# Kernel tuning notes

Hardware: AMD Instinct MI355X
Metric: run time of the kernel (lower is better)

## Reference

```python
import jax, jax.numpy as jnp
import numpy as np

N_NODES = 100000
N_EDGES = 1600000
NODE_DIM = 64
EDGE_DIM = 16
HIDDEN_DIM = 64


def setup_inputs() -> dict:
    key = jax.random.key(0)
    ks = jax.random.split(key, 9)
    x = jax.random.normal(ks[0], (N_NODES, NODE_DIM), dtype=jnp.float32)
    edge_index = jax.random.randint(ks[1], (2, N_EDGES), 0, N_NODES, dtype=jnp.int32)
    edge_attr = jax.random.normal(ks[2], (N_EDGES, EDGE_DIM), dtype=jnp.float32)
    msg_in = 2 * NODE_DIM + EDGE_DIM
    s1 = 1.0 / np.sqrt(msg_in)
    s2 = 1.0 / np.sqrt(HIDDEN_DIM)
    su = 1.0 / np.sqrt(NODE_DIM + HIDDEN_DIM)
    W1 = jax.random.uniform(ks[3], (msg_in, HIDDEN_DIM), jnp.float32, -s1, s1)
    b1 = jax.random.uniform(ks[4], (HIDDEN_DIM,), jnp.float32, -s1, s1)
    W2 = jax.random.uniform(ks[5], (HIDDEN_DIM, HIDDEN_DIM), jnp.float32, -s2, s2)
    b2 = jax.random.uniform(ks[6], (HIDDEN_DIM,), jnp.float32, -s2, s2)
    Wu = jax.random.uniform(ks[7], (NODE_DIM + HIDDEN_DIM, NODE_DIM), jnp.float32, -su, su)
    bu = jax.random.uniform(ks[8], (NODE_DIM,), jnp.float32, -su, su)
    return {"x": x, "edge_index": edge_index, "edge_attr": edge_attr,
            "W1": W1, "b1": b1, "W2": W2, "b2": b2, "Wu": Wu, "bu": bu}


def reference(x, edge_index, edge_attr, W1, b1, W2, b2, Wu, bu):
    src, dst = edge_index[0], edge_index[1]
    n_nodes = x.shape[0]
    # gather endpoint features + edge features -> (E, 2*node_dim+edge_dim)
    edge_input = jnp.concatenate([x[src], x[dst], edge_attr], axis=1)
    # message MLP (dropout is identity in eval mode)
    h = jax.nn.relu(edge_input @ W1 + b1)
    messages = h @ W2 + b2  # (E, hidden)
    # scatter-add to dst, count-normalize (mean aggregation)
    aggregated = jax.ops.segment_sum(messages, dst, num_segments=n_nodes)
    counts = jax.ops.segment_sum(jnp.ones((messages.shape[0], 1), x.dtype), dst,
                                 num_segments=n_nodes)
    aggregated = aggregated / (counts + 1e-6)
    # update MLP + residual
    update_input = jnp.concatenate([x, aggregated], axis=1)
    x_new = jax.nn.relu(update_input @ Wu + bu)
    return x + x_new
```

## Files before the change

### kernel.cpp

```cpp
#include <hip/hip_runtime.h>

#define N_NODES  100000
#define N_EDGES  1600000
#define NODE_DIM 64
#define EDGE_DIM 16
#define HIDDEN   64
#define N_GROUPS 100000
#define EDGE_BLOCKS 768

typedef __bf16 bf16x8 __attribute__((ext_vector_type(8)));
typedef unsigned short u16x8 __attribute__((ext_vector_type(8)));
typedef unsigned short u16x4 __attribute__((ext_vector_type(4)));
typedef float f32x4 __attribute__((ext_vector_type(4)));
typedef float f32x2 __attribute__((ext_vector_type(2)));

__device__ __forceinline__ unsigned short f2bf(float f) {
    unsigned int u = __float_as_uint(f);
    u += 0x7FFFu + ((u >> 16) & 1u);
    return (unsigned short)(u >> 16);
}

__device__ __forceinline__ float bf2f(unsigned short s) {
    return __uint_as_float((unsigned int)s << 16);
}

__device__ __forceinline__ bf16x8 lds_frag(const unsigned short* p) {
    return __builtin_bit_cast(bf16x8, *(const u16x8*)p);
}

__device__ __forceinline__ void cvt16v(unsigned short* dst,
                                       float4 f0, float4 f1, float4 f2, float4 f3) {
    u16x8 p0, p1;
    p0[0]=f2bf(f0.x); p0[1]=f2bf(f0.y); p0[2]=f2bf(f0.z); p0[3]=f2bf(f0.w);
    p0[4]=f2bf(f1.x); p0[5]=f2bf(f1.y); p0[6]=f2bf(f1.z); p0[7]=f2bf(f1.w);
    p1[0]=f2bf(f2.x); p1[1]=f2bf(f2.y); p1[2]=f2bf(f2.z); p1[3]=f2bf(f2.w);
    p1[4]=f2bf(f3.x); p1[5]=f2bf(f3.y); p1[6]=f2bf(f3.z); p1[7]=f2bf(f3.w);
    *(u16x8*)dst       = p0;
    *(u16x8*)(dst + 8) = p1;
}

__device__ __forceinline__ void cvt4v(unsigned short* dst, float4 f) {
    u16x4 p;
    p[0]=f2bf(f.x); p[1]=f2bf(f.y); p[2]=f2bf(f.z); p[3]=f2bf(f.w);
    *(u16x4*)dst = p;
}

__device__ __forceinline__ void atomic_pk_add_bf16(unsigned short* p, unsigned int v) {
    asm volatile("global_atomic_pk_add_bf16 %0, %1, off"
                 :: "v"(p), "v"(v) : "memory");
}

__global__ void prep_kernel(const float* __restrict__ W1, const float* __restrict__ W2,
                            const float* __restrict__ Wu, const float* __restrict__ x,
                            unsigned short* __restrict__ W1t,
                            unsigned short* __restrict__ W2t,
                            unsigned short* __restrict__ Wut,
                            unsigned short* __restrict__ xb)
{
    int t = blockIdx.x * 256 + threadIdx.x;
    int stride = gridDim.x * 256;
    for (int i = t; i < N_NODES * 64 / 4; i += stride) {
        float4 f = ((const float4*)x)[i];
        cvt4v(&xb[i * 4], f);
    }
    for (int i = t; i < 64 * 160; i += stride) {
        int n = i / 160, k = i % 160;
        W1t[i] = (k < 144) ? f2bf(W1[k * 64 + n]) : (unsigned short)0;
    }
    for (int i = t; i < 64 * 64; i += stride) {
        int n = i / 64, k = i % 64;
        W2t[i] = f2bf(W2[k * 64 + n]);
    }
    for (int i = t; i < 64 * 128; i += stride) {
        int n = i / 128, k = i % 128;
        Wut[i] = f2bf(Wu[k * 64 + n]);
    }
}

#define SA  168
#define SW1 164
#define SH  72
#define WAVE_LDS (16*SA*2 + 16*SH*2)

__global__ __launch_bounds__(256, 3) void edge_kernel(
    const unsigned short* __restrict__ xb,
    const int*   __restrict__ ei,
    const float* __restrict__ ea,
    const unsigned short* __restrict__ W1t,
    const unsigned short* __restrict__ W2t,
    const float* __restrict__ b1,
    const float* __restrict__ b2,
    unsigned short* __restrict__ agg,
    float* __restrict__ cnt)
{
    __shared__ __align__(16) unsigned short sW1[64 * SW1];
    __shared__ __align__(16) unsigned char  sAH[4 * WAVE_LDS];
    __shared__ int sdst[64];

    const int t    = threadIdx.x;
    const int lane = t & 63;
    const int w    = t >> 6;

    #pragma unroll
    for (int i = 0; i < 5; i++) {
        int c = t + i * 256;
        int n = c / 20, k8 = c % 20;
        *(u16x8*)&sW1[n * SW1 + k8 * 8] = *(const u16x8*)&W1t[c * 8];
    }
    __syncthreads();

    unsigned short* myAin = (unsigned short*)(sAH + w * WAVE_LDS);
    float*          myMsg = (float*)myAin;
    unsigned short* myH   = (unsigned short*)(sAH + w * WAVE_LDS + 16 * SA * 2);

    if (lane < 16) {
        u16x8 z = {0,0,0,0,0,0,0,0};
        *(u16x8*)&myAin[lane * SA + 144] = z;
        *(u16x8*)&myAin[lane * SA + 152] = z;
    }

    const int col = lane & 15;
    const int kq  = lane >> 4;
    const int el  = lane >> 2;
    const int q   = lane & 3;
    const int c2  = lane & 31;
    const int eh  = lane >> 5;

    float b1r[4], b2r[4];
    u16x8 w2f[8];
    #pragma unroll
    for (int ct = 0; ct < 4; ct++) {
        b1r[ct] = b1[ct * 16 + col];
        b2r[ct] = b2[ct * 16 + col];
        #pragma unroll
        for (int ks = 0; ks < 2; ks++)
            w2f[ks * 4 + ct] = *(const u16x8*)&W2t[(ct * 16 + col) * 64 + ks * 32 + kq * 8];
    }

    const int TW = EDGE_BLOCKS * 4;
    const int gw = blockIdx.x * 4 + w;

    int d_cur;
    u16x8 gx[4];
    float4 fe;
    {
        int e = gw * 16 + el;
        int s = ei[e];
        d_cur = ei[N_EDGES + e];
        const u16x8* ps = (const u16x8*)(xb + (size_t)s * 64);
        const u16x8* pd = (const u16x8*)(xb + (size_t)d_cur * 64);
        gx[0] = ps[2 * q]; gx[1] = ps[2 * q + 1];
        gx[2] = pd[2 * q]; gx[3] = pd[2 * q + 1];
        fe = ((const float4*)ea)[(size_t)gw * 64 + lane];
    }

    for (int g = gw; g < N_GROUPS; g += TW) {
        const int gn = g + TW;
        const bool more = gn < N_GROUPS;
        int sn = 0, dn = 0;
        if (more) {
            int e2 = gn * 16 + el;
            sn = ei[e2];
            dn = ei[N_EDGES + e2];
        }

        unsigned short* row = myAin + el * SA;
        *(u16x8*)(row + q * 16)          = gx[0];
        *(u16x8*)(row + q * 16 + 8)      = gx[1];
        *(u16x8*)(row + 64 + q * 16)     = gx[2];
        *(u16x8*)(row + 64 + q * 16 + 8) = gx[3];
        cvt4v(&row[128 + q * 4], fe);
        if (q == 1) sdst[w * 16 + el] = d_cur;
        if (q == 2) atomicAdd(&cnt[d_cur], 1.0f);

        if (more) {
            const u16x8* ps = (const u16x8*)(xb + (size_t)sn * 64);
            const u16x8* pd = (const u16x8*)(xb + (size_t)dn * 64);
            gx[0] = ps[2 * q]; gx[1] = ps[2 * q + 1];
            gx[2] = pd[2 * q]; gx[3] = pd[2 * q + 1];
            fe = ((const float4*)ea)[(size_t)gn * 64 + lane];
        }
        d_cur = dn;

        __builtin_amdgcn_wave_barrier();

        f32x4 acc[4] = {{0,0,0,0},{0,0,0,0},{0,0,0,0},{0,0,0,0}};
        #pragma unroll
        for (int ks = 0; ks < 5; ks++) {
            int ko = ks * 32 + kq * 8;
            bf16x8 a = lds_frag(&myAin[col * SA + ko]);
            #pragma unroll
            for (int ct = 0; ct < 4; ct++) {
                bf16x8 b = lds_frag(&sW1[(ct * 16 + col) * SW1 + ko]);
                acc[ct] = __builtin_amdgcn_mfma_f32_16x16x32_bf16(a, b, acc[ct], 0, 0, 0);
            }
        }
        #pragma unroll
        for (int ct = 0; ct < 4; ct++) {
            #pragma unroll
            for (int r = 0; r < 4; r++)
                myH[(kq * 4 + r) * SH + ct * 16 + col] =
                    f2bf(fmaxf(acc[ct][r] + b1r[ct], 0.0f));
        }
        __builtin_amdgcn_wave_barrier();

        f32x4 m[4] = {{0,0,0,0},{0,0,0,0},{0,0,0,0},{0,0,0,0}};
        #pragma unroll
        for (int ks = 0; ks < 2; ks++) {
            int ko = ks * 32 + kq * 8;
            bf16x8 a = lds_frag(&myH[col * SH + ko]);
            #pragma unroll
            for (int ct = 0; ct < 4; ct++)
                m[ct] = __builtin_amdgcn_mfma_f32_16x16x32_bf16(
                    a, __builtin_bit_cast(bf16x8, w2f[ks * 4 + ct]), m[ct], 0, 0, 0);
        }
        #pragma unroll
        for (int ct = 0; ct < 4; ct++) {
            #pragma unroll
            for (int r = 0; r < 4; r++)
                myMsg[(kq * 4 + r) * 84 + ct * 16 + col] = m[ct][r] + b2r[ct];
        }
        __builtin_amdgcn_wave_barrier();

        #pragma unroll 1
        for (int i = 0; i < 8; i++) {
            int   el2 = i * 2 + eh;
            int   dd  = sdst[w * 16 + el2];
            f32x2 v   = *(const f32x2*)&myMsg[el2 * 84 + c2 * 2];
            unsigned int pk = ((unsigned int)f2bf(v[1]) << 16) | f2bf(v[0]);
            atomic_pk_add_bf16(&agg[(size_t)dd * 64 + c2 * 2], pk);
        }
        __builtin_amdgcn_wave_barrier();
    }
}

#define NSA 136
__global__ __launch_bounds__(256, 4) void node_kernel(
    const float* __restrict__ x,
    const unsigned short* __restrict__ agg,
    const float* __restrict__ cnt,
    const unsigned short* __restrict__ Wut,
    const float* __restrict__ bu,
    float* __restrict__ out)
{
    __shared__ __align__(16) unsigned short sA [64 * NSA];
    __shared__ __align__(16) unsigned short sWu[64 * NSA];
    const int t = threadIdx.x, lane = t & 63, w = t >> 6;
    const int n0 = blockIdx.x * 64;

    #pragma unroll
    for (int i = 0; i < 4; i++) {
        int c = t + i * 256;
        int n = c / 16, k8 = c % 16;
        *(u16x8*)&sWu[n * NSA + k8 * 8] = *(const u16x8*)&Wut[c * 8];
    }
    {
        const int nl = t >> 2, q = t & 3;
        const int n = n0 + nl;
        unsigned short* row = sA + nl * NSA;
        if (n < N_NODES) {
            const float4* px = (const float4*)(x + (size_t)n * 64);
            cvt16v(row + q * 16, px[q*4], px[q*4+1], px[q*4+2], px[q*4+3]);
            float inv = 1.0f / (cnt[n] + 1e-6f);
            const u16x8* pa = (const u16x8*)(agg + (size_t)n * 64);
            u16x8 a0 = pa[2 * q], a1 = pa[2 * q + 1];
            u16x8 r0, r1;
            #pragma unroll
            for (int j = 0; j < 8; j++) {
                r0[j] = f2bf(bf2f(a0[j]) * inv);
                r1[j] = f2bf(bf2f(a1[j]) * inv);
            }
            *(u16x8*)(row + 64 + q * 16)     = r0;
            *(u16x8*)(row + 64 + q * 16 + 8) = r1;
        } else {
            u16x8 z = {0,0,0,0,0,0,0,0};
            *(u16x8*)&row[q * 16]          = z;
            *(u16x8*)&row[q * 16 + 8]      = z;
            *(u16x8*)&row[64 + q * 16]     = z;
            *(u16x8*)&row[64 + q * 16 + 8] = z;
        }
    }
    __syncthreads();

    const int col = lane & 15, kq = lane >> 4;
    const int arow = w * 16 + col;
    f32x4 acc[4] = {{0,0,0,0},{0,0,0,0},{0,0,0,0},{0,0,0,0}};
    #pragma unroll
    for (int ks = 0; ks < 4; ks++) {
        int ko = ks * 32 + kq * 8;
        bf16x8 a = lds_frag(&sA[arow * NSA + ko]);
        #pragma unroll
        for (int ct = 0; ct < 4; ct++) {
            bf16x8 b = lds_frag(&sWu[(ct * 16 + col) * NSA + ko]);
            acc[ct] = __builtin_amdgcn_mfma_f32_16x16x32_bf16(a, b, acc[ct], 0, 0, 0);
        }
    }
    #pragma unroll
    for (int ct = 0; ct < 4; ct++) {
        float bb = bu[ct * 16 + col];
        #pragma unroll
        for (int r = 0; r < 4; r++) {
            int row = w * 16 + kq * 4 + r;
            int n = n0 + row;
            if (n < N_NODES) {
                int c2 = ct * 16 + col;
                float xa = x[(size_t)n * 64 + c2];
                out[(size_t)n * 64 + c2] = xa + fmaxf(acc[ct][r] + bb, 0.0f);
            }
        }
    }
}

extern "C" void kernel_launch(void* const* d_in, const int* in_sizes, int n_in,
                              void* d_out, int out_size, void* d_ws, size_t ws_size,
                              hipStream_t stream) {
    const float* x  = (const float*)d_in[0];
    const int*   ei = (const int*)  d_in[1];
    const float* ea = (const float*)d_in[2];
    const float* W1 = (const float*)d_in[3];
    const float* b1 = (const float*)d_in[4];
    const float* W2 = (const float*)d_in[5];
    const float* b2 = (const float*)d_in[6];
    const float* Wu = (const float*)d_in[7];
    const float* bu = (const float*)d_in[8];
    float* out = (float*)d_out;

    unsigned short* agg = (unsigned short*)d_ws;
    float* cnt = (float*)(agg + (size_t)N_NODES * HIDDEN);
    unsigned short* W1t = (unsigned short*)(cnt + N_NODES);
    unsigned short* W2t = W1t + 64 * 160;
    unsigned short* Wut = W2t + 64 * 64;
    unsigned short* xb  = Wut + 64 * 128;

    hipMemsetAsync(d_ws, 0,
                   (size_t)N_NODES * HIDDEN * sizeof(unsigned short)
                   + (size_t)N_NODES * sizeof(float), stream);

    prep_kernel<<<512, 256, 0, stream>>>(W1, W2, Wu, x, W1t, W2t, Wut, xb);
    edge_kernel<<<EDGE_BLOCKS, 256, 0, stream>>>(xb, ei, ea, W1t, W2t, b1, b2, agg, cnt);
    node_kernel<<<(N_NODES + 63) / 64, 256, 0, stream>>>(x, agg, cnt, Wut, bu, out);
}
```

Measured before the change: 469.8 us.

## Keep edge MLP in registers via transposed MFMA and fold biases

Rewrites the edge kernel to compute the message MLP as W^T·X, with gathered node features fed straight from registers as MFMA B operands. This removes the per-wave LDS staging of inputs, hidden activations and messages. b1 is folded into W1 through a constant-one padding column, and b2 is moved to the node kernel, where it is applied once per node that has incoming edges. The kernel also prefetches two groups ahead and raises occupancy (launch bounds 5, 1280 blocks). In exchange it issues more atomics per lane with smaller per-row locality, and it rounds b1 to bf16.

```diff
diff --git a/kernel.cpp b/kernel.cpp
--- a/kernel.cpp
+++ b/kernel.cpp
@@ -6,13 +6,13 @@
 #define EDGE_DIM 16
 #define HIDDEN   64
 #define N_GROUPS 100000
-#define EDGE_BLOCKS 768
+#define EDGE_BLOCKS 1280
 
 typedef __bf16 bf16x8 __attribute__((ext_vector_type(8)));
 typedef unsigned short u16x8 __attribute__((ext_vector_type(8)));
 typedef unsigned short u16x4 __attribute__((ext_vector_type(4)));
+typedef unsigned int   u32x4 __attribute__((ext_vector_type(4)));
 typedef float f32x4 __attribute__((ext_vector_type(4)));
-typedef float f32x2 __attribute__((ext_vector_type(2)));
 
 __device__ __forceinline__ unsigned short f2bf(float f) {
     unsigned int u = __float_as_uint(f);
@@ -26,6 +26,10 @@
 
 __device__ __forceinline__ bf16x8 lds_frag(const unsigned short* p) {
     return __builtin_bit_cast(bf16x8, *(const u16x8*)p);
+}
+
+__device__ __forceinline__ unsigned pk2(float lo, float hi) {
+    return ((unsigned)f2bf(hi) << 16) | (unsigned)f2bf(lo);
 }
 
 __device__ __forceinline__ void cvt16v(unsigned short* dst,
@@ -50,8 +54,9 @@
                  :: "v"(p), "v"(v) : "memory");
 }
 
-__global__ void prep_kernel(const float* __restrict__ W1, const float* __restrict__ W2,
-                            const float* __restrict__ Wu, const float* __restrict__ x,
+__global__ void prep_kernel(const float* __restrict__ W1, const float* __restrict__ b1,
+                            const float* __restrict__ W2, const float* __restrict__ Wu,
+                            const float* __restrict__ x,
                             unsigned short* __restrict__ W1t,
                             unsigned short* __restrict__ W2t,
                             unsigned short* __restrict__ Wut,
@@ -65,7 +70,8 @@
     }
     for (int i = t; i < 64 * 160; i += stride) {
         int n = i / 160, k = i % 160;
-        W1t[i] = (k < 144) ? f2bf(W1[k * 64 + n]) : (unsigned short)0;
+        float v = (k < 144) ? W1[k * 64 + n] : (k == 144 ? b1[n] : 0.0f);
+        W1t[i] = f2bf(v);
     }
     for (int i = t; i < 64 * 64; i += stride) {
         int n = i / 64, k = i % 64;
@@ -77,25 +83,23 @@
     }
 }
 
-#define SA  168
 #define SW1 164
-#define SH  72
-#define WAVE_LDS (16*SA*2 + 16*SH*2)
-
-__global__ __launch_bounds__(256, 3) void edge_kernel(
+#define SW2 66
+
+#define MFMA_BF16 __builtin_amdgcn_mfma_f32_16x16x32_bf16
+#define BC(v) __builtin_bit_cast(bf16x8, v)
+
+__global__ __launch_bounds__(256, 5) void edge_kernel(
     const unsigned short* __restrict__ xb,
     const int*   __restrict__ ei,
     const float* __restrict__ ea,
     const unsigned short* __restrict__ W1t,
     const unsigned short* __restrict__ W2t,
-    const float* __restrict__ b1,
-    const float* __restrict__ b2,
     unsigned short* __restrict__ agg,
     float* __restrict__ cnt)
 {
     __shared__ __align__(16) unsigned short sW1[64 * SW1];
-    __shared__ __align__(16) unsigned char  sAH[4 * WAVE_LDS];
-    __shared__ int sdst[64];
+    __shared__ __align__(16) unsigned short sW2[64 * SW2];
 
     const int t    = threadIdx.x;
     const int lane = t & 63;
@@ -104,133 +108,123 @@
     #pragma unroll
     for (int i = 0; i < 5; i++) {
         int c = t + i * 256;
-        int n = c / 20, k8 = c % 20;
-        *(u16x8*)&sW1[n * SW1 + k8 * 8] = *(const u16x8*)&W1t[c * 8];
+        int row16 = c / 20, chunk = c % 20;
+        int ct = row16 >> 4, ii = row16 & 15;
+        int srcRow = ((ii >> 2) << 3) + (ct & 1) * 32 + ((ct >> 1) << 2) + (ii & 3);
+        *(u16x8*)&sW1[row16 * SW1 + chunk * 8] = *(const u16x8*)&W1t[srcRow * 160 + chunk * 8];
+    }
+    #pragma unroll
+    for (int i = 0; i < 2; i++) {
+        int c = t + i * 256;
+        int n = c >> 3, k8 = c & 7;
+        *(u16x8*)&sW2[n * SW2 + k8 * 8] = *(const u16x8*)&W2t[n * 64 + k8 * 8];
     }
     __syncthreads();
-
-    unsigned short* myAin = (unsigned short*)(sAH + w * WAVE_LDS);
-    float*          myMsg = (float*)myAin;
-    unsigned short* myH   = (unsigned short*)(sAH + w * WAVE_LDS + 16 * SA * 2);
-
-    if (lane < 16) {
-        u16x8 z = {0,0,0,0,0,0,0,0};
-        *(u16x8*)&myAin[lane * SA + 144] = z;
-        *(u16x8*)&myAin[lane * SA + 152] = z;
-    }
 
     const int col = lane & 15;
     const int kq  = lane >> 4;
-    const int el  = lane >> 2;
-    const int q   = lane & 3;
-    const int c2  = lane & 31;
-    const int eh  = lane >> 5;
-
-    float b1r[4], b2r[4];
-    u16x8 w2f[8];
-    #pragma unroll
-    for (int ct = 0; ct < 4; ct++) {
-        b1r[ct] = b1[ct * 16 + col];
-        b2r[ct] = b2[ct * 16 + col];
-        #pragma unroll
-        for (int ks = 0; ks < 2; ks++)
-            w2f[ks * 4 + ct] = *(const u16x8*)&W2t[(ct * 16 + col) * 64 + ks * 32 + kq * 8];
-    }
+
+    u16x8 padf = {0,0,0,0,0,0,0,0};
+    if (kq == 2) padf[0] = 0x3F80;
 
     const int TW = EDGE_BLOCKS * 4;
-    const int gw = blockIdx.x * 4 + w;
-
-    int d_cur;
-    u16x8 gx[4];
-    float4 fe;
-    {
-        int e = gw * 16 + el;
-        int s = ei[e];
-        d_cur = ei[N_EDGES + e];
-        const u16x8* ps = (const u16x8*)(xb + (size_t)s * 64);
-        const u16x8* pd = (const u16x8*)(xb + (size_t)d_cur * 64);
-        gx[0] = ps[2 * q]; gx[1] = ps[2 * q + 1];
-        gx[2] = pd[2 * q]; gx[3] = pd[2 * q + 1];
-        fe = ((const float4*)ea)[(size_t)gw * 64 + lane];
-    }
-
-    for (int g = gw; g < N_GROUPS; g += TW) {
-        const int gn = g + TW;
-        const bool more = gn < N_GROUPS;
-        int sn = 0, dn = 0;
-        if (more) {
-            int e2 = gn * 16 + el;
-            sn = ei[e2];
-            dn = ei[N_EDGES + e2];
-        }
-
-        unsigned short* row = myAin + el * SA;
-        *(u16x8*)(row + q * 16)          = gx[0];
-        *(u16x8*)(row + q * 16 + 8)      = gx[1];
-        *(u16x8*)(row + 64 + q * 16)     = gx[2];
-        *(u16x8*)(row + 64 + q * 16 + 8) = gx[3];
-        cvt4v(&row[128 + q * 4], fe);
-        if (q == 1) sdst[w * 16 + el] = d_cur;
-        if (q == 2) atomicAdd(&cnt[d_cur], 1.0f);
-
-        if (more) {
-            const u16x8* ps = (const u16x8*)(xb + (size_t)sn * 64);
-            const u16x8* pd = (const u16x8*)(xb + (size_t)dn * 64);
-            gx[0] = ps[2 * q]; gx[1] = ps[2 * q + 1];
-            gx[2] = pd[2 * q]; gx[3] = pd[2 * q + 1];
-            fe = ((const float4*)ea)[(size_t)gn * 64 + lane];
-        }
-        d_cur = dn;
-
-        __builtin_amdgcn_wave_barrier();
-
-        f32x4 acc[4] = {{0,0,0,0},{0,0,0,0},{0,0,0,0},{0,0,0,0}};
-        #pragma unroll
-        for (int ks = 0; ks < 5; ks++) {
-            int ko = ks * 32 + kq * 8;
-            bf16x8 a = lds_frag(&myAin[col * SA + ko]);
-            #pragma unroll
-            for (int ct = 0; ct < 4; ct++) {
-                bf16x8 b = lds_frag(&sW1[(ct * 16 + col) * SW1 + ko]);
-                acc[ct] = __builtin_amdgcn_mfma_f32_16x16x32_bf16(a, b, acc[ct], 0, 0, 0);
-            }
-        }
-        #pragma unroll
-        for (int ct = 0; ct < 4; ct++) {
-            #pragma unroll
-            for (int r = 0; r < 4; r++)
-                myH[(kq * 4 + r) * SH + ct * 16 + col] =
-                    f2bf(fmaxf(acc[ct][r] + b1r[ct], 0.0f));
-        }
-        __builtin_amdgcn_wave_barrier();
-
-        f32x4 m[4] = {{0,0,0,0},{0,0,0,0},{0,0,0,0},{0,0,0,0}};
-        #pragma unroll
-        for (int ks = 0; ks < 2; ks++) {
-            int ko = ks * 32 + kq * 8;
-            bf16x8 a = lds_frag(&myH[col * SH + ko]);
-            #pragma unroll
-            for (int ct = 0; ct < 4; ct++)
-                m[ct] = __builtin_amdgcn_mfma_f32_16x16x32_bf16(
-                    a, __builtin_bit_cast(bf16x8, w2f[ks * 4 + ct]), m[ct], 0, 0, 0);
-        }
-        #pragma unroll
-        for (int ct = 0; ct < 4; ct++) {
-            #pragma unroll
-            for (int r = 0; r < 4; r++)
-                myMsg[(kq * 4 + r) * 84 + ct * 16 + col] = m[ct][r] + b2r[ct];
-        }
-        __builtin_amdgcn_wave_barrier();
-
-        #pragma unroll 1
-        for (int i = 0; i < 8; i++) {
-            int   el2 = i * 2 + eh;
-            int   dd  = sdst[w * 16 + el2];
-            f32x2 v   = *(const f32x2*)&myMsg[el2 * 84 + c2 * 2];
-            unsigned int pk = ((unsigned int)f2bf(v[1]) << 16) | f2bf(v[0]);
-            atomic_pk_add_bf16(&agg[(size_t)dd * 64 + c2 * 2], pk);
-        }
-        __builtin_amdgcn_wave_barrier();
+    int g = blockIdx.x * 4 + w;
+
+    int eiv  = ei[g * 16 + col + ((lane & 16) ? N_EDGES : 0)];
+    int srcI = __shfl(eiv, col);
+    int dstI = __shfl(eiv, 16 + col);
+    const u16x8* ps = (const u16x8*)(xb + (size_t)srcI * 64);
+    u16x8 sf0 = ps[kq], sf1 = ps[4 + kq];
+    const u16x8* pd = (const u16x8*)(xb + (size_t)dstI * 64);
+    u16x8 df0 = pd[kq], df1 = pd[4 + kq];
+    float4 ea0 = {0,0,0,0}, ea1 = {0,0,0,0};
+    if (kq < 2) {
+        const float4* pe = (const float4*)(ea + ((size_t)g * 16 + col) * 16 + kq * 8);
+        ea0 = pe[0]; ea1 = pe[1];
+    }
+    int gn  = g + TW;
+    int gln = (gn < N_GROUPS) ? gn : g;
+    int eivN = ei[gln * 16 + col + ((lane & 16) ? N_EDGES : 0)];
+
+    for (;;) {
+        int srcN = __shfl(eivN, col);
+        int dstN = __shfl(eivN, 16 + col);
+        const u16x8* psN = (const u16x8*)(xb + (size_t)srcN * 64);
+        u16x8 sfN0 = psN[kq], sfN1 = psN[4 + kq];
+        const u16x8* pdN = (const u16x8*)(xb + (size_t)dstN * 64);
+        u16x8 dfN0 = pdN[kq], dfN1 = pdN[4 + kq];
+        float4 eaN0 = {0,0,0,0}, eaN1 = {0,0,0,0};
+        if (kq < 2) {
+            const float4* pe = (const float4*)(ea + ((size_t)gln * 16 + col) * 16 + kq * 8);
+            eaN0 = pe[0]; eaN1 = pe[1];
+        }
+        int gn2  = gn + TW;
+        int gln2 = (gn2 < N_GROUPS) ? gn2 : gln;
+        int eivN2 = ei[gln2 * 16 + col + ((lane & 16) ? N_EDGES : 0)];
+
+        u16x8 ef;
+        ef[0]=f2bf(ea0.x); ef[1]=f2bf(ea0.y); ef[2]=f2bf(ea0.z); ef[3]=f2bf(ea0.w);
+        ef[4]=f2bf(ea1.x); ef[5]=f2bf(ea1.y); ef[6]=f2bf(ea1.z); ef[7]=f2bf(ea1.w);
+        u16x8 b4u = (kq < 2) ? ef : padf;
+
+        f32x4 a0={0,0,0,0}, a1={0,0,0,0}, a2={0,0,0,0}, a3={0,0,0,0};
+        #define G1STEP(KS, BB)                                                        \
+        {   int ko = (KS) * 32 + kq * 8;                                              \
+            a0 = MFMA_BF16(lds_frag(&sW1[( 0 + col) * SW1 + ko]), BC(BB), a0, 0,0,0); \
+            a1 = MFMA_BF16(lds_frag(&sW1[(16 + col) * SW1 + ko]), BC(BB), a1, 0,0,0); \
+            a2 = MFMA_BF16(lds_frag(&sW1[(32 + col) * SW1 + ko]), BC(BB), a2, 0,0,0); \
+            a3 = MFMA_BF16(lds_frag(&sW1[(48 + col) * SW1 + ko]), BC(BB), a3, 0,0,0); \
+        }
+        G1STEP(0, sf0)
+        G1STEP(1, sf1)
+        G1STEP(2, df0)
+        G1STEP(3, df1)
+        G1STEP(4, b4u)
+        #undef G1STEP
+
+        unsigned p0 = pk2(fmaxf(a0[0],0.f), fmaxf(a0[1],0.f));
+        unsigned p1 = pk2(fmaxf(a0[2],0.f), fmaxf(a0[3],0.f));
+        unsigned p2 = pk2(fmaxf(a1[0],0.f), fmaxf(a1[1],0.f));
+        unsigned p3 = pk2(fmaxf(a1[2],0.f), fmaxf(a1[3],0.f));
+        unsigned p4 = pk2(fmaxf(a2[0],0.f), fmaxf(a2[1],0.f));
+        unsigned p5 = pk2(fmaxf(a2[2],0.f), fmaxf(a2[3],0.f));
+        unsigned p6 = pk2(fmaxf(a3[0],0.f), fmaxf(a3[1],0.f));
+        unsigned p7 = pk2(fmaxf(a3[2],0.f), fmaxf(a3[3],0.f));
+        u32x4 h0v = {p0, p1, p4, p5};
+        u32x4 h1v = {p2, p3, p6, p7};
+        bf16x8 hf0 = __builtin_bit_cast(bf16x8, h0v);
+        bf16x8 hf1 = __builtin_bit_cast(bf16x8, h1v);
+
+        f32x4 m0={0,0,0,0}, m1={0,0,0,0}, m2={0,0,0,0}, m3={0,0,0,0};
+        {
+            int ko = kq * 8;
+            m0 = MFMA_BF16(lds_frag(&sW2[( 0 + col) * SW2 + ko]), hf0, m0, 0,0,0);
+            m1 = MFMA_BF16(lds_frag(&sW2[(16 + col) * SW2 + ko]), hf0, m1, 0,0,0);
+            m2 = MFMA_BF16(lds_frag(&sW2[(32 + col) * SW2 + ko]), hf0, m2, 0,0,0);
+            m3 = MFMA_BF16(lds_frag(&sW2[(48 + col) * SW2 + ko]), hf0, m3, 0,0,0);
+            ko += 32;
+            m0 = MFMA_BF16(lds_frag(&sW2[( 0 + col) * SW2 + ko]), hf1, m0, 0,0,0);
+            m1 = MFMA_BF16(lds_frag(&sW2[(16 + col) * SW2 + ko]), hf1, m1, 0,0,0);
+            m2 = MFMA_BF16(lds_frag(&sW2[(32 + col) * SW2 + ko]), hf1, m2, 0,0,0);
+            m3 = MFMA_BF16(lds_frag(&sW2[(48 + col) * SW2 + ko]), hf1, m3, 0,0,0);
+        }
+
+        unsigned short* bp = agg + (size_t)dstI * 64 + kq * 4;
+        atomic_pk_add_bf16(bp +  0, pk2(m0[0], m0[1]));
+        atomic_pk_add_bf16(bp +  2, pk2(m0[2], m0[3]));
+        atomic_pk_add_bf16(bp + 16, pk2(m1[0], m1[1]));
+        atomic_pk_add_bf16(bp + 18, pk2(m1[2], m1[3]));
+        atomic_pk_add_bf16(bp + 32, pk2(m2[0], m2[1]));
+        atomic_pk_add_bf16(bp + 34, pk2(m2[2], m2[3]));
+        atomic_pk_add_bf16(bp + 48, pk2(m3[0], m3[1]));
+        atomic_pk_add_bf16(bp + 50, pk2(m3[2], m3[3]));
+        if (lane < 16) atomicAdd(&cnt[dstI], 1.0f);
+
+        if (gn >= N_GROUPS) break;
+        g = gn; gn = gn2; gln = gln2;
+        sf0 = sfN0; sf1 = sfN1; df0 = dfN0; df1 = dfN1;
+        ea0 = eaN0; ea1 = eaN1; dstI = dstN;
+        eiv = eivN; eivN = eivN2;
     }
 }
 
@@ -241,6 +235,7 @@
     const float* __restrict__ cnt,
     const unsigned short* __restrict__ Wut,
     const float* __restrict__ bu,
+    const float* __restrict__ b2,
     float* __restrict__ out)
 {
     __shared__ __align__(16) unsigned short sA [64 * NSA];
@@ -261,14 +256,16 @@
         if (n < N_NODES) {
             const float4* px = (const float4*)(x + (size_t)n * 64);
             cvt16v(row + q * 16, px[q*4], px[q*4+1], px[q*4+2], px[q*4+3]);
-            float inv = 1.0f / (cnt[n] + 1e-6f);
+            float cv  = cnt[n];
+            float inv = 1.0f / (cv + 1e-6f);
+            float hasb = (cv > 0.5f) ? 1.0f : 0.0f;
             const u16x8* pa = (const u16x8*)(agg + (size_t)n * 64);
             u16x8 a0 = pa[2 * q], a1 = pa[2 * q + 1];
             u16x8 r0, r1;
             #pragma unroll
             for (int j = 0; j < 8; j++) {
-                r0[j] = f2bf(bf2f(a0[j]) * inv);
-                r1[j] = f2bf(bf2f(a1[j]) * inv);
+                r0[j] = f2bf(bf2f(a0[j]) * inv + hasb * b2[q * 16 + j]);
+                r1[j] = f2bf(bf2f(a1[j]) * inv + hasb * b2[q * 16 + 8 + j]);
             }
             *(u16x8*)(row + 64 + q * 16)     = r0;
             *(u16x8*)(row + 64 + q * 16 + 8) = r1;
@@ -292,7 +289,7 @@
         #pragma unroll
         for (int ct = 0; ct < 4; ct++) {
             bf16x8 b = lds_frag(&sWu[(ct * 16 + col) * NSA + ko]);
-            acc[ct] = __builtin_amdgcn_mfma_f32_16x16x32_bf16(a, b, acc[ct], 0, 0, 0);
+            acc[ct] = MFMA_BF16(a, b, acc[ct], 0, 0, 0);
         }
     }
     #pragma unroll
@@ -336,7 +333,7 @@
                    (size_t)N_NODES * HIDDEN * sizeof(unsigned short)
                    + (size_t)N_NODES * sizeof(float), stream);
 
-    prep_kernel<<<512, 256, 0, stream>>>(W1, W2, Wu, x, W1t, W2t, Wut, xb);
-    edge_kernel<<<EDGE_BLOCKS, 256, 0, stream>>>(xb, ei, ea, W1t, W2t, b1, b2, agg, cnt);
-    node_kernel<<<(N_NODES + 63) / 64, 256, 0, stream>>>(x, agg, cnt, Wut, bu, out);
-}
+    prep_kernel<<<512, 256, 0, stream>>>(W1, b1, W2, Wu, x, W1t, W2t, Wut, xb);
+    edge_kernel<<<EDGE_BLOCKS, 256, 0, stream>>>(xb, ei, ea, W1t, W2t, agg, cnt);
+    node_kernel<<<(N_NODES + 63) / 64, 256, 0, stream>>>(x, agg, cnt, Wut, bu, b2, out);
+}
```

After: 929.7 us. 1.98x slower.
